# Optimization experiments

Measured on AMD Instinct MI355X. Metric: run time of the kernel, lower is better.

The kernel has to match this reference:

```python
import jax, jax.numpy as jnp
import numpy as np

NUM_THETAS = 64   # bump_steps == num_thetas == 64
NUM_PTS = 100
B = 256           # number of graphs
N = B * NUM_PTS   # total nodes
SCALE = 500.0     # sigmoid sharpness used by EctLayer
HID = 4 * 1024


def _linear_init(key, fan_in, shape):
    s = 1.0 / np.sqrt(fan_in)
    return jax.random.uniform(key, shape, jnp.float32, -s, s)


def setup_inputs() -> dict:
    key = jax.random.key(0)
    ks = jax.random.split(key, 8)
    x = jax.random.normal(ks[0], (N, 2), jnp.float32)
    batch_idx = jnp.repeat(jnp.arange(B), NUM_PTS)  # [N] graph id per node
    t = jnp.linspace(0.0, 2.0 * np.pi, NUM_THETAS)
    V = jnp.stack([jnp.sin(t), jnp.cos(t)], axis=0)          # [2, T] directions
    lin = jnp.linspace(-1.0, 1.0, NUM_THETAS)                # [bump] thresholds
    d = NUM_THETAS * NUM_THETAS
    W1 = _linear_init(ks[1], d, (d, HID)); b1 = _linear_init(ks[2], d, (HID,))
    W2 = _linear_init(ks[3], HID, (HID, HID)); b2 = _linear_init(ks[4], HID, (HID,))
    W3 = _linear_init(ks[5], HID, (HID, 2 * NUM_PTS)); b3 = _linear_init(ks[6], HID, (2 * NUM_PTS,))
    return {"x": x, "batch_idx": batch_idx, "V": V, "lin": lin,
            "W1": W1, "b1": b1, "W2": W2, "b2": b2, "W3": W3, "b3": b3}


def ect_layer(x, idx, V, lin, num_graphs):
    # x: [N,2], V: [2,T] -> node heights nh: [N,T]
    nh = x @ V
    # soft-threshold binning: [N, bump, T]
    ecc = jax.nn.sigmoid(SCALE * (lin[None, :, None] - nh[:, None, :]))
    # per-graph scatter-sum over nodes -> [B, bump, T]
    e = jax.ops.segment_sum(ecc, idx, num_segments=num_graphs)
    # normalized=True: divide by per-graph max
    return e / jnp.amax(e, axis=(1, 2), keepdims=True)


def reference(x, batch_idx, V, lin, W1, b1, W2, b2, W3, b3):
    ect = ect_layer(x, batch_idx, V, lin, B)          # [B, 64, 64]
    h = ect.reshape(B, -1)                            # Flatten
    h = jnp.tanh(h @ W1 + b1)
    h = jnp.tanh(h @ W2 + b2)
    pts = (h @ W3 + b3).reshape(-1, 2)                # [B*NUM_PTS, 2]
    idx2 = jnp.repeat(jnp.arange(B), NUM_PTS)
    decoded = ect_layer(pts, idx2, V, lin, B)         # [B, 64, 64]
    return decoded, pts
```

## Files before the change

### kernel.cpp

```cpp
#include <hip/hip_runtime.h>
#include <hip/hip_bf16.h>

typedef short bf16x8 __attribute__((ext_vector_type(8)));
typedef short s16x4 __attribute__((ext_vector_type(4)));
typedef float f32x4 __attribute__((ext_vector_type(4)));
typedef unsigned u32x4 __attribute__((ext_vector_type(4)));

#define ECT_SCALE 500.0f

__device__ __forceinline__ bool detect_f32(const void* w) {
    const unsigned* p = (const unsigned*)w;
    int sane = 0;
#pragma unroll
    for (int i = 0; i < 16; i++) {
        unsigned e = (p[i] >> 7) & 0xFFu;
        sane += (e >= 100u && e <= 140u) ? 1 : 0;
    }
    return sane < 10;
}

__device__ __forceinline__ float ld_f(const void* p, int i, bool f32) {
    return f32 ? ((const float*)p)[i]
               : __bfloat162float(((const __hip_bfloat16*)p)[i]);
}

__device__ __forceinline__ void split_f(float v, short& hi, short& lo) {
    __hip_bfloat16 h = __float2bfloat16(v);
    hi = (short)__bfloat16_as_short(h);
    lo = (short)__bfloat16_as_short(__float2bfloat16(v - __bfloat162float(h)));
}

__device__ __forceinline__ float sig_fast(float x) {
    float t = __builtin_amdgcn_fmed3f(x, 0.0f, 1.0f);
    return t * t * (3.0f - 2.0f * t);
}

__global__ __launch_bounds__(512)
void ect1_kernel(const void* __restrict__ x, const void* __restrict__ V,
                 const void* __restrict__ lin, const void* __restrict__ sent,
                 short* __restrict__ eh, short* __restrict__ el)
{
    __shared__ float in_lds[200];
    __shared__ float nh[100 * 64];
    __shared__ float wmax[8];

    const bool f32 = detect_f32(sent);
    const int g = blockIdx.x, tid = threadIdx.x;
    const int t = tid & 63, wv = tid >> 6;

    if (tid < 200) in_lds[tid] = ld_f(x, g * 200 + tid, f32);
    const float sv = ld_f(V, t, f32);
    const float cv = ld_f(V, 64 + t, f32);
    float zs[8];
#pragma unroll
    for (int k = 0; k < 8; k++)
        zs[k] = (ECT_SCALE / 8.0f) * ld_f(lin, wv + 8 * k, f32) + 0.5f;
    __syncthreads();

    for (int n = wv; n < 100; n += 8)
        nh[n * 64 + t] = in_lds[2 * n] * sv + in_lds[2 * n + 1] * cv;

    float e[8];
#pragma unroll
    for (int k = 0; k < 8; k++) e[k] = 0.0f;
    __syncthreads();

    for (int n = 0; n < 100; n++) {
        const float ws = (ECT_SCALE / 8.0f) * nh[n * 64 + t];
#pragma unroll
        for (int k = 0; k < 8; k++)
            e[k] += sig_fast(zs[k] - ws);
    }

    float mx = e[0];
#pragma unroll
    for (int k = 1; k < 8; k++) mx = fmaxf(mx, e[k]);
#pragma unroll
    for (int off = 32; off > 0; off >>= 1)
        mx = fmaxf(mx, __shfl_xor(mx, off, 64));
    if (t == 0) wmax[wv] = mx;
    __syncthreads();
    float gm = wmax[0];
#pragma unroll
    for (int k = 1; k < 8; k++) gm = fmaxf(gm, wmax[k]);
    const float sc = 1.0f / gm;

#pragma unroll
    for (int k = 0; k < 8; k++) {
        short hi, lo;
        split_f(e[k] * sc, hi, lo);
        eh[g * 4096 + tid + 512 * k] = hi;
        el[g * 4096 + tid + 512 * k] = lo;
    }
}

#define GEMM_STAGE(K_, N_, GUARD_N)                                            \
    {                                                                          \
        _Pragma("unroll")                                                      \
        for (int i = 0; i < 2; i++) {                                          \
            int r = rr + 32 * i;                                               \
            *(bf16x8*)&Ahs[r][cc] =                                            \
                *(const bf16x8*)&Ah[(size_t)(bm * 64 + r) * K_ + k0 + cc];     \
            *(bf16x8*)&Als[r][cc] =                                            \
                *(const bf16x8*)&Al[(size_t)(bm * 64 + r) * K_ + k0 + cc];     \
        }                                                                      \
        {                                                                      \
            const int wn = lane;                                               \
            const int wk = wv * 16;                                            \
            const bool okn = !(GUARD_N) || (n0c + wn < N_);                    \
            unsigned hp[8], lp[8];                                             \
            if (f32) {                                                         \
                float w0[16];                                                  \
                _Pragma("unroll")                                              \
                for (int j = 0; j < 16; j++)                                   \
                    w0[j] = okn ? ((const float*)W)[(size_t)(k0 + wk + j) * N_ + n0c + wn] : 0.0f; \
                _Pragma("unroll")                                              \
                for (int jp = 0; jp < 8; jp++) {                               \
                    unsigned ua = __float_as_uint(w0[2 * jp]);                 \
                    unsigned ub = __float_as_uint(w0[2 * jp + 1]);             \
                    unsigned ha = ua & 0xFFFF0000u, hb = ub & 0xFFFF0000u;     \
                    hp[jp] = (ha >> 16) | hb;                                  \
                    float la = w0[2 * jp] - __uint_as_float(ha);               \
                    float lb = w0[2 * jp + 1] - __uint_as_float(hb);           \
                    lp[jp] = (__float_as_uint(la) >> 16) |                     \
                             (__float_as_uint(lb) & 0xFFFF0000u);              \
                }                                                              \
            } else {                                                           \
                unsigned short wu[16];                                         \
                _Pragma("unroll")                                              \
                for (int j = 0; j < 16; j++)                                   \
                    wu[j] = okn ? ((const unsigned short*)W)[(size_t)(k0 + wk + j) * N_ + n0c + wn] : (unsigned short)0; \
                _Pragma("unroll")                                              \
                for (int jp = 0; jp < 8; jp++) {                               \
                    hp[jp] = (unsigned)wu[2 * jp] | ((unsigned)wu[2 * jp + 1] << 16); \
                    lp[jp] = 0u;                                               \
                }                                                              \
            }                                                                  \
            *(u32x4*)&Bhs[wn][wk]     = (u32x4){hp[0], hp[1], hp[2], hp[3]};   \
            *(u32x4*)&Bhs[wn][wk + 8] = (u32x4){hp[4], hp[5], hp[6], hp[7]};   \
            *(u32x4*)&Bls[wn][wk]     = (u32x4){lp[0], lp[1], lp[2], lp[3]};   \
            *(u32x4*)&Bls[wn][wk + 8] = (u32x4){lp[4], lp[5], lp[6], lp[7]};   \
        }                                                                      \
        __syncthreads();                                                       \
        _Pragma("unroll")                                                      \
        for (int kh = 0; kh < 2; kh++) {                                       \
            bf16x8 ah[2], al[2], bh[2], bl[2];                                 \
            _Pragma("unroll")                                                  \
            for (int im = 0; im < 2; im++) {                                   \
                ah[im] = *(const bf16x8*)&Ahs[mrow0 + im * 16 + l16][kh * 32 + quad * 8]; \
                al[im] = *(const bf16x8*)&Als[mrow0 + im * 16 + l16][kh * 32 + quad * 8]; \
            }                                                                  \
            _Pragma("unroll")                                                  \
            for (int jn = 0; jn < 2; jn++) {                                   \
                bh[jn] = *(const bf16x8*)&Bhs[ncol0 + jn * 16 + l16][kh * 32 + quad * 8]; \
                bl[jn] = *(const bf16x8*)&Bls[ncol0 + jn * 16 + l16][kh * 32 + quad * 8]; \
            }                                                                  \
            _Pragma("unroll")                                                  \
            for (int im = 0; im < 2; im++)                                     \
                _Pragma("unroll")                                              \
                for (int jn = 0; jn < 2; jn++) {                               \
                    acc[im][jn] = __builtin_amdgcn_mfma_f32_16x16x32_bf16(ah[im], bh[jn], acc[im][jn], 0, 0, 0); \
                    acc[im][jn] = __builtin_amdgcn_mfma_f32_16x16x32_bf16(ah[im], bl[jn], acc[im][jn], 0, 0, 0); \
                    acc[im][jn] = __builtin_amdgcn_mfma_f32_16x16x32_bf16(al[im], bh[jn], acc[im][jn], 0, 0, 0); \
                }                                                              \
        }                                                                      \
        __syncthreads();                                                       \
    }

template<bool GUARD>
__global__ __launch_bounds__(256)
void gemm_sk(const short* __restrict__ Ah, const short* __restrict__ Al,
             const void* __restrict__ W, const void* __restrict__ sent,
             float* __restrict__ pre, int N_, int K_, int kzbits, int kiters)
{
    __shared__ short Ahs[64][72], Als[64][72], Bhs[64][72], Bls[64][72];
    const bool f32 = detect_f32(sent);
    const int bm = blockIdx.y;
    const int bn = blockIdx.x >> kzbits;
    const int kz = blockIdx.x & ((1 << kzbits) - 1);
    const int tid = threadIdx.x;
    const int wv = tid >> 6, lane = tid & 63, quad = lane >> 4, l16 = lane & 15;
    const int mrow0 = (wv & 1) * 32, ncol0 = (wv >> 1) * 32;
    const int rr = tid >> 3, cc = (tid & 7) * 8;
    const int n0c = bn * 64;

    f32x4 acc[2][2];
#pragma unroll
    for (int i = 0; i < 2; i++)
#pragma unroll
        for (int j = 0; j < 2; j++) acc[i][j] = (f32x4){0.f, 0.f, 0.f, 0.f};

    int k0 = kz * (kiters * 64);
    for (int it = 0; it < kiters; it++, k0 += 64)
        GEMM_STAGE(K_, N_, GUARD)

#pragma unroll
    for (int im = 0; im < 2; im++)
#pragma unroll
        for (int jn = 0; jn < 2; jn++) {
            const int n = n0c + ncol0 + jn * 16 + l16;
            if (!GUARD || n < N_) {
#pragma unroll
                for (int r = 0; r < 4; r++) {
                    const int m = bm * 64 + mrow0 + im * 16 + quad * 4 + r;
                    atomicAdd(&pre[(size_t)m * N_ + n], acc[im][jn][r]);
                }
            }
        }
}

__global__ __launch_bounds__(256)
void finalize_tanh(const float* __restrict__ pre, const void* __restrict__ bias,
                   const void* __restrict__ sent,
                   short* __restrict__ Oh, short* __restrict__ Ol)
{
    const bool f32 = detect_f32(sent);
    const int idx = (blockIdx.x * 256 + threadIdx.x) * 4;
    f32x4 v = *(const f32x4*)&pre[idx];
    const int n = idx & 4095;
    s16x4 hi, lo;
#pragma unroll
    for (int j = 0; j < 4; j++) {
        float t = v[j] + ld_f(bias, n + j, f32);
        t = 1.0f - 2.0f * __builtin_amdgcn_rcpf(1.0f + __expf(2.0f * t));
        short h, l;
        split_f(t, h, l);
        hi[j] = h; lo[j] = l;
    }
    *(s16x4*)&Oh[idx] = hi;
    *(s16x4*)&Ol[idx] = lo;
}

__global__ __launch_bounds__(512)
void ect2_kernel(const float* __restrict__ part, const void* __restrict__ bias3,
                 const void* __restrict__ V, const void* __restrict__ lin,
                 const void* __restrict__ sent,
                 float* __restrict__ dec, float* __restrict__ pts_out)
{
    __shared__ float in_lds[200];
    __shared__ float nh[100 * 64];
    __shared__ float wmax[8];

    const bool f32 = detect_f32(sent);
    const int g = blockIdx.x, tid = threadIdx.x;
    const int t = tid & 63, wv = tid >> 6;

    if (tid < 200) {
        float v = part[g * 200 + tid] + ld_f(bias3, tid, f32);
        in_lds[tid] = v;
        pts_out[g * 200 + tid] = v;
    }
    const float sv = ld_f(V, t, f32);
    const float cv = ld_f(V, 64 + t, f32);
    float zs[8];
#pragma unroll
    for (int k = 0; k < 8; k++)
        zs[k] = (ECT_SCALE / 8.0f) * ld_f(lin, wv + 8 * k, f32) + 0.5f;
    __syncthreads();

    for (int n = wv; n < 100; n += 8)
        nh[n * 64 + t] = in_lds[2 * n] * sv + in_lds[2 * n + 1] * cv;

    float e[8];
#pragma unroll
    for (int k = 0; k < 8; k++) e[k] = 0.0f;
    __syncthreads();

    for (int n = 0; n < 100; n++) {
        const float ws = (ECT_SCALE / 8.0f) * nh[n * 64 + t];
#pragma unroll
        for (int k = 0; k < 8; k++)
            e[k] += sig_fast(zs[k] - ws);
    }

    float mx = e[0];
#pragma unroll
    for (int k = 1; k < 8; k++) mx = fmaxf(mx, e[k]);
#pragma unroll
    for (int off = 32; off > 0; off >>= 1)
        mx = fmaxf(mx, __shfl_xor(mx, off, 64));
    if (t == 0) wmax[wv] = mx;
    __syncthreads();
    float gm = wmax[0];
#pragma unroll
    for (int k = 1; k < 8; k++) gm = fmaxf(gm, wmax[k]);
    const float sc = 1.0f / gm;

#pragma unroll
    for (int k = 0; k < 8; k++)
        dec[g * 4096 + tid + 512 * k] = e[k] * sc;
}

extern "C" void kernel_launch(void* const* d_in, const int* in_sizes, int n_in,
                              void* d_out, int out_size, void* d_ws, size_t ws_size,
                              hipStream_t stream)
{
    const void* x   = d_in[0];
    const void* V   = d_in[2];
    const void* lin = d_in[3];
    const void* W1  = d_in[4];
    const void* b1  = d_in[5];
    const void* W2  = d_in[6];
    const void* b2  = d_in[7];
    const void* W3  = d_in[8];
    const void* b3  = d_in[9];
    float* out = (float*)d_out;

    char* ws = (char*)d_ws;
    short* e_h  = (short*)(ws + ( 0u << 20));
    short* e_l  = (short*)(ws + ( 2u << 20));
    short* h1h  = (short*)(ws + ( 4u << 20));
    short* h1l  = (short*)(ws + ( 6u << 20));
    short* h2h  = (short*)(ws + ( 8u << 20));
    short* h2l  = (short*)(ws + (10u << 20));
    float* pre1 = (float*)(ws + (12u << 20));
    float* pre2 = (float*)(ws + (16u << 20));
    float* part = (float*)(ws + (20u << 20));

    hipMemsetAsync(ws + (12u << 20), 0, (8u << 20) + 256 * 200 * sizeof(float), stream);

    ect1_kernel<<<256, 512, 0, stream>>>(x, V, lin, W1, e_h, e_l);
    gemm_sk<false><<<dim3(256, 4), 256, 0, stream>>>(e_h, e_l, W1, W1, pre1, 4096, 4096, 2, 16);
    finalize_tanh<<<1024, 256, 0, stream>>>(pre1, b1, W1, h1h, h1l);
    gemm_sk<false><<<dim3(256, 4), 256, 0, stream>>>(h1h, h1l, W2, W1, pre2, 4096, 4096, 2, 16);
    finalize_tanh<<<1024, 256, 0, stream>>>(pre2, b2, W1, h2h, h2l);
    gemm_sk<true><<<dim3(128, 4), 256, 0, stream>>>(h2h, h2l, W3, W1, part, 200, 4096, 5, 2);
    ect2_kernel<<<256, 512, 0, stream>>>(part, b3, V, lin, W1, out, out + 1048576);
}
```

Measured before the change: 278.1 us.

## Fuse whole pipeline into one cooperative persistent kernel with grid syncs

Replaces the seven separate launches and the memset with a single cooperative kernel of 256 blocks that runs the ECT, the three GEMMs, the tanh finalization and the decode ECT as phases separated by grid.sync. The GEMMs move to larger 256x128 tiles with double-buffered LDS and register prefetch, and write split-K partial slices to distinct buffers that a later phase sums, instead of using atomics. This removes launch gaps, atomic traffic and the zeroing memset. In exchange it runs only 256 blocks across the device, relies on grid-wide barriers, uses about 123 KB of dynamic LDS, and needs more workspace for the partial slices.

Measured after the change: 463.8 us. 1.67x slower.

```diff
diff --git a/kernel.cpp b/kernel.cpp
--- a/kernel.cpp
+++ b/kernel.cpp
@@ -1,8 +1,10 @@
 #include <hip/hip_runtime.h>
 #include <hip/hip_bf16.h>
+#include <hip/hip_cooperative_groups.h>
+
+namespace cg = cooperative_groups;
 
 typedef short bf16x8 __attribute__((ext_vector_type(8)));
-typedef short s16x4 __attribute__((ext_vector_type(4)));
 typedef float f32x4 __attribute__((ext_vector_type(4)));
 typedef unsigned u32x4 __attribute__((ext_vector_type(4)));
 
@@ -35,20 +37,22 @@
     return t * t * (3.0f - 2.0f * t);
 }
 
-__global__ __launch_bounds__(512)
-void ect1_kernel(const void* __restrict__ x, const void* __restrict__ V,
-                 const void* __restrict__ lin, const void* __restrict__ sent,
-                 short* __restrict__ eh, short* __restrict__ el)
-{
-    __shared__ float in_lds[200];
-    __shared__ float nh[100 * 64];
-    __shared__ float wmax[8];
-
-    const bool f32 = detect_f32(sent);
-    const int g = blockIdx.x, tid = threadIdx.x;
+#define AHS(b, r, k) ah_lds[((b) * 256 + (r)) * 40 + (k)]
+#define ALS(b, r, k) al_lds[((b) * 256 + (r)) * 40 + (k)]
+#define BHS(b, n, k) bh_lds[((b) * 128 + (n)) * 40 + (k)]
+#define BLS(b, n, k) bl_lds[((b) * 128 + (n)) * 40 + (k)]
+
+template<bool SPLIT_OUT>
+__device__ void ect_core(char* smem, const void* V, const void* lin, bool f32,
+                         int g, int tid,
+                         short* eh, short* el, float* dec)
+{
+    float* in_lds = (float*)smem;
+    float* nh     = (float*)(smem + 1024);
+    float* wmax   = (float*)(smem + 27008);
+
     const int t = tid & 63, wv = tid >> 6;
 
-    if (tid < 200) in_lds[tid] = ld_f(x, g * 200 + tid, f32);
     const float sv = ld_f(V, t, f32);
     const float cv = ld_f(V, 64 + t, f32);
     float zs[8];
@@ -87,208 +91,207 @@
 
 #pragma unroll
     for (int k = 0; k < 8; k++) {
-        short hi, lo;
-        split_f(e[k] * sc, hi, lo);
-        eh[g * 4096 + tid + 512 * k] = hi;
-        el[g * 4096 + tid + 512 * k] = lo;
-    }
-}
-
-#define GEMM_STAGE(K_, N_, GUARD_N)                                            \
+        if (SPLIT_OUT) {
+            short hi, lo;
+            split_f(e[k] * sc, hi, lo);
+            eh[g * 4096 + tid + 512 * k] = hi;
+            el[g * 4096 + tid + 512 * k] = lo;
+        } else {
+            dec[g * 4096 + tid + 512 * k] = e[k] * sc;
+        }
+    }
+}
+
+template<bool GUARD>
+__device__ void gemm_phase(char* smem, const short* Ah, const short* Al,
+                           const void* W, bool f32, int N_,
+                           int bn, int kz, int niter,
+                           float* slice, int tid)
+{
+    short* ah_lds = (short*)smem;
+    short* al_lds = (short*)(smem + 40960);
+    short* bh_lds = (short*)(smem + 81920);
+    short* bl_lds = (short*)(smem + 102400);
+
+    const int wv = tid >> 6, lane = tid & 63, quad = lane >> 4, l16 = lane & 15;
+    const int wm = (wv & 3) * 64, wn = (wv >> 2) * 64;
+    const int ar0 = tid >> 2, ac = (tid & 3) * 8;
+    const int sub = wv & 1, ksl = wv >> 1;
+    const int nn = sub * 64 + lane - sub * 64;
+    const int nloc = sub * 64 + (lane & 63);
+    const int gn = bn * 128 + nloc;
+    const int k0base = kz * (niter * 32);
+
+    f32x4 acc[4][4];
+#pragma unroll
+    for (int i = 0; i < 4; i++)
+#pragma unroll
+        for (int j = 0; j < 4; j++) acc[i][j] = (f32x4){0.f, 0.f, 0.f, 0.f};
+
+    bf16x8 pah[2], pal[2];
+    unsigned pw[8];
+
+#define PF(k0_)                                                                \
     {                                                                          \
         _Pragma("unroll")                                                      \
-        for (int i = 0; i < 2; i++) {                                          \
-            int r = rr + 32 * i;                                               \
-            *(bf16x8*)&Ahs[r][cc] =                                            \
-                *(const bf16x8*)&Ah[(size_t)(bm * 64 + r) * K_ + k0 + cc];     \
-            *(bf16x8*)&Als[r][cc] =                                            \
-                *(const bf16x8*)&Al[(size_t)(bm * 64 + r) * K_ + k0 + cc];     \
+        for (int p = 0; p < 2; p++) {                                          \
+            int r = ar0 + 128 * p;                                             \
+            pah[p] = *(const bf16x8*)&Ah[(size_t)r * 4096 + (k0_) + ac];       \
+            pal[p] = *(const bf16x8*)&Al[(size_t)r * 4096 + (k0_) + ac];       \
         }                                                                      \
-        {                                                                      \
-            const int wn = lane;                                               \
-            const int wk = wv * 16;                                            \
-            const bool okn = !(GUARD_N) || (n0c + wn < N_);                    \
-            unsigned hp[8], lp[8];                                             \
-            if (f32) {                                                         \
-                float w0[16];                                                  \
-                _Pragma("unroll")                                              \
-                for (int j = 0; j < 16; j++)                                   \
-                    w0[j] = okn ? ((const float*)W)[(size_t)(k0 + wk + j) * N_ + n0c + wn] : 0.0f; \
-                _Pragma("unroll")                                              \
-                for (int jp = 0; jp < 8; jp++) {                               \
-                    unsigned ua = __float_as_uint(w0[2 * jp]);                 \
-                    unsigned ub = __float_as_uint(w0[2 * jp + 1]);             \
-                    unsigned ha = ua & 0xFFFF0000u, hb = ub & 0xFFFF0000u;     \
-                    hp[jp] = (ha >> 16) | hb;                                  \
-                    float la = w0[2 * jp] - __uint_as_float(ha);               \
-                    float lb = w0[2 * jp + 1] - __uint_as_float(hb);           \
-                    lp[jp] = (__float_as_uint(la) >> 16) |                     \
-                             (__float_as_uint(lb) & 0xFFFF0000u);              \
-                }                                                              \
-            } else {                                                           \
-                unsigned short wu[16];                                         \
-                _Pragma("unroll")                                              \
-                for (int j = 0; j < 16; j++)                                   \
-                    wu[j] = okn ? ((const unsigned short*)W)[(size_t)(k0 + wk + j) * N_ + n0c + wn] : (unsigned short)0; \
-                _Pragma("unroll")                                              \
-                for (int jp = 0; jp < 8; jp++) {                               \
-                    hp[jp] = (unsigned)wu[2 * jp] | ((unsigned)wu[2 * jp + 1] << 16); \
-                    lp[jp] = 0u;                                               \
-                }                                                              \
-            }                                                                  \
-            *(u32x4*)&Bhs[wn][wk]     = (u32x4){hp[0], hp[1], hp[2], hp[3]};   \
-            *(u32x4*)&Bhs[wn][wk + 8] = (u32x4){hp[4], hp[5], hp[6], hp[7]};   \
-            *(u32x4*)&Bls[wn][wk]     = (u32x4){lp[0], lp[1], lp[2], lp[3]};   \
-            *(u32x4*)&Bls[wn][wk + 8] = (u32x4){lp[4], lp[5], lp[6], lp[7]};   \
+        _Pragma("unroll")                                                      \
+        for (int j = 0; j < 8; j++) {                                          \
+            size_t off = (size_t)((k0_) + ksl * 8 + j) * N_ + gn;              \
+            pw[j] = (GUARD && gn >= N_) ? 0u                                   \
+                  : (f32 ? ((const unsigned*)W)[off]                           \
+                         : ((unsigned)((const unsigned short*)W)[off] << 16)); \
         }                                                                      \
-        __syncthreads();                                                       \
+    }
+
+#define WRITE(buf_)                                                            \
+    {                                                                          \
         _Pragma("unroll")                                                      \
-        for (int kh = 0; kh < 2; kh++) {                                       \
-            bf16x8 ah[2], al[2], bh[2], bl[2];                                 \
-            _Pragma("unroll")                                                  \
-            for (int im = 0; im < 2; im++) {                                   \
-                ah[im] = *(const bf16x8*)&Ahs[mrow0 + im * 16 + l16][kh * 32 + quad * 8]; \
-                al[im] = *(const bf16x8*)&Als[mrow0 + im * 16 + l16][kh * 32 + quad * 8]; \
-            }                                                                  \
-            _Pragma("unroll")                                                  \
-            for (int jn = 0; jn < 2; jn++) {                                   \
-                bh[jn] = *(const bf16x8*)&Bhs[ncol0 + jn * 16 + l16][kh * 32 + quad * 8]; \
-                bl[jn] = *(const bf16x8*)&Bls[ncol0 + jn * 16 + l16][kh * 32 + quad * 8]; \
-            }                                                                  \
-            _Pragma("unroll")                                                  \
-            for (int im = 0; im < 2; im++)                                     \
-                _Pragma("unroll")                                              \
-                for (int jn = 0; jn < 2; jn++) {                               \
-                    acc[im][jn] = __builtin_amdgcn_mfma_f32_16x16x32_bf16(ah[im], bh[jn], acc[im][jn], 0, 0, 0); \
-                    acc[im][jn] = __builtin_amdgcn_mfma_f32_16x16x32_bf16(ah[im], bl[jn], acc[im][jn], 0, 0, 0); \
-                    acc[im][jn] = __builtin_amdgcn_mfma_f32_16x16x32_bf16(al[im], bh[jn], acc[im][jn], 0, 0, 0); \
-                }                                                              \
+        for (int p = 0; p < 2; p++) {                                          \
+            *(bf16x8*)&AHS(buf_, ar0 + 128 * p, ac) = pah[p];                  \
+            *(bf16x8*)&ALS(buf_, ar0 + 128 * p, ac) = pal[p];                  \
         }                                                                      \
-        __syncthreads();                                                       \
-    }
-
-template<bool GUARD>
-__global__ __launch_bounds__(256)
-void gemm_sk(const short* __restrict__ Ah, const short* __restrict__ Al,
-             const void* __restrict__ W, const void* __restrict__ sent,
-             float* __restrict__ pre, int N_, int K_, int kzbits, int kiters)
-{
-    __shared__ short Ahs[64][72], Als[64][72], Bhs[64][72], Bls[64][72];
-    const bool f32 = detect_f32(sent);
-    const int bm = blockIdx.y;
-    const int bn = blockIdx.x >> kzbits;
-    const int kz = blockIdx.x & ((1 << kzbits) - 1);
-    const int tid = threadIdx.x;
-    const int wv = tid >> 6, lane = tid & 63, quad = lane >> 4, l16 = lane & 15;
-    const int mrow0 = (wv & 1) * 32, ncol0 = (wv >> 1) * 32;
-    const int rr = tid >> 3, cc = (tid & 7) * 8;
-    const int n0c = bn * 64;
-
-    f32x4 acc[2][2];
-#pragma unroll
-    for (int i = 0; i < 2; i++)
-#pragma unroll
-        for (int j = 0; j < 2; j++) acc[i][j] = (f32x4){0.f, 0.f, 0.f, 0.f};
-
-    int k0 = kz * (kiters * 64);
-    for (int it = 0; it < kiters; it++, k0 += 64)
-        GEMM_STAGE(K_, N_, GUARD)
-
-#pragma unroll
-    for (int im = 0; im < 2; im++)
-#pragma unroll
-        for (int jn = 0; jn < 2; jn++) {
-            const int n = n0c + ncol0 + jn * 16 + l16;
+        unsigned hp[4], lp[4];                                                 \
+        _Pragma("unroll")                                                      \
+        for (int jp = 0; jp < 4; jp++) {                                       \
+            unsigned a = pw[2 * jp], b = pw[2 * jp + 1];                       \
+            unsigned ha = a & 0xFFFF0000u, hb = b & 0xFFFF0000u;               \
+            hp[jp] = (ha >> 16) | hb;                                          \
+            float la = __uint_as_float(a) - __uint_as_float(ha);               \
+            float lb = __uint_as_float(b) - __uint_as_float(hb);               \
+            lp[jp] = (__float_as_uint(la) >> 16) |                             \
+                     (__float_as_uint(lb) & 0xFFFF0000u);                      \
+        }                                                                      \
+        *(u32x4*)&BHS(buf_, nloc, ksl * 8) = (u32x4){hp[0], hp[1], hp[2], hp[3]}; \
+        *(u32x4*)&BLS(buf_, nloc, ksl * 8) = (u32x4){lp[0], lp[1], lp[2], lp[3]}; \
+    }
+
+    PF(k0base)
+    WRITE(0)
+    __syncthreads();
+    PF(k0base + 32)
+
+    for (int it = 0; it < niter; it++) {
+        const int b = it & 1;
+        bf16x8 afh[4], afl[4], bfh[4], bfl[4];
+#pragma unroll
+        for (int i = 0; i < 4; i++) {
+            afh[i] = *(const bf16x8*)&AHS(b, wm + i * 16 + l16, quad * 8);
+            afl[i] = *(const bf16x8*)&ALS(b, wm + i * 16 + l16, quad * 8);
+        }
+#pragma unroll
+        for (int j = 0; j < 4; j++) {
+            bfh[j] = *(const bf16x8*)&BHS(b, wn + j * 16 + l16, quad * 8);
+            bfl[j] = *(const bf16x8*)&BLS(b, wn + j * 16 + l16, quad * 8);
+        }
+#pragma unroll
+        for (int i = 0; i < 4; i++)
+#pragma unroll
+            for (int j = 0; j < 4; j++) {
+                acc[i][j] = __builtin_amdgcn_mfma_f32_16x16x32_bf16(afh[i], bfh[j], acc[i][j], 0, 0, 0);
+                acc[i][j] = __builtin_amdgcn_mfma_f32_16x16x32_bf16(afh[i], bfl[j], acc[i][j], 0, 0, 0);
+                acc[i][j] = __builtin_amdgcn_mfma_f32_16x16x32_bf16(afl[i], bfh[j], acc[i][j], 0, 0, 0);
+            }
+        if (it + 1 < niter) WRITE((it + 1) & 1)
+        __syncthreads();
+        if (it + 2 < niter) PF(k0base + (it + 2) * 32)
+    }
+
+#pragma unroll
+    for (int i = 0; i < 4; i++)
+#pragma unroll
+        for (int j = 0; j < 4; j++) {
+            const int n = bn * 128 + wn + j * 16 + l16;
             if (!GUARD || n < N_) {
 #pragma unroll
                 for (int r = 0; r < 4; r++) {
-                    const int m = bm * 64 + mrow0 + im * 16 + quad * 4 + r;
-                    atomicAdd(&pre[(size_t)m * N_ + n], acc[im][jn][r]);
+                    const int m = wm + i * 16 + quad * 4 + r;
+                    slice[(size_t)m * N_ + n] = acc[i][j][r];
                 }
             }
         }
-}
-
-__global__ __launch_bounds__(256)
-void finalize_tanh(const float* __restrict__ pre, const void* __restrict__ bias,
-                   const void* __restrict__ sent,
-                   short* __restrict__ Oh, short* __restrict__ Ol)
-{
-    const bool f32 = detect_f32(sent);
-    const int idx = (blockIdx.x * 256 + threadIdx.x) * 4;
-    f32x4 v = *(const f32x4*)&pre[idx];
+#undef PF
+#undef WRITE
+}
+
+__device__ void finalize_phase(const float* pre, const void* bias, bool f32,
+                               short* Oh, short* Ol, int bid, int tid)
+{
+    const int idx = (bid * 512 + tid) * 8;
+    f32x4 s0 = (f32x4){0.f, 0.f, 0.f, 0.f}, s1 = s0;
+#pragma unroll
+    for (int z = 0; z < 8; z++) {
+        s0 += *(const f32x4*)&pre[(size_t)z * 1048576 + idx];
+        s1 += *(const f32x4*)&pre[(size_t)z * 1048576 + idx + 4];
+    }
     const int n = idx & 4095;
-    s16x4 hi, lo;
-#pragma unroll
-    for (int j = 0; j < 4; j++) {
-        float t = v[j] + ld_f(bias, n + j, f32);
-        t = 1.0f - 2.0f * __builtin_amdgcn_rcpf(1.0f + __expf(2.0f * t));
+    bf16x8 hi, lo;
+#pragma unroll
+    for (int j = 0; j < 8; j++) {
+        float v = (j < 4 ? s0[j & 3] : s1[j & 3]) + ld_f(bias, n + j, f32);
+        v = 1.0f - 2.0f * __builtin_amdgcn_rcpf(1.0f + __expf(2.0f * v));
         short h, l;
-        split_f(t, h, l);
+        split_f(v, h, l);
         hi[j] = h; lo[j] = l;
     }
-    *(s16x4*)&Oh[idx] = hi;
-    *(s16x4*)&Ol[idx] = lo;
+    *(bf16x8*)&Oh[idx] = hi;
+    *(bf16x8*)&Ol[idx] = lo;
 }
 
 __global__ __launch_bounds__(512)
-void ect2_kernel(const float* __restrict__ part, const void* __restrict__ bias3,
-                 const void* __restrict__ V, const void* __restrict__ lin,
-                 const void* __restrict__ sent,
-                 float* __restrict__ dec, float* __restrict__ pts_out)
-{
-    __shared__ float in_lds[200];
-    __shared__ float nh[100 * 64];
-    __shared__ float wmax[8];
-
-    const bool f32 = detect_f32(sent);
-    const int g = blockIdx.x, tid = threadIdx.x;
-    const int t = tid & 63, wv = tid >> 6;
-
-    if (tid < 200) {
-        float v = part[g * 200 + tid] + ld_f(bias3, tid, f32);
-        in_lds[tid] = v;
-        pts_out[g * 200 + tid] = v;
-    }
-    const float sv = ld_f(V, t, f32);
-    const float cv = ld_f(V, 64 + t, f32);
-    float zs[8];
-#pragma unroll
-    for (int k = 0; k < 8; k++)
-        zs[k] = (ECT_SCALE / 8.0f) * ld_f(lin, wv + 8 * k, f32) + 0.5f;
-    __syncthreads();
-
-    for (int n = wv; n < 100; n += 8)
-        nh[n * 64 + t] = in_lds[2 * n] * sv + in_lds[2 * n + 1] * cv;
-
-    float e[8];
-#pragma unroll
-    for (int k = 0; k < 8; k++) e[k] = 0.0f;
-    __syncthreads();
-
-    for (int n = 0; n < 100; n++) {
-        const float ws = (ECT_SCALE / 8.0f) * nh[n * 64 + t];
-#pragma unroll
-        for (int k = 0; k < 8; k++)
-            e[k] += sig_fast(zs[k] - ws);
-    }
-
-    float mx = e[0];
-#pragma unroll
-    for (int k = 1; k < 8; k++) mx = fmaxf(mx, e[k]);
-#pragma unroll
-    for (int off = 32; off > 0; off >>= 1)
-        mx = fmaxf(mx, __shfl_xor(mx, off, 64));
-    if (t == 0) wmax[wv] = mx;
-    __syncthreads();
-    float gm = wmax[0];
-#pragma unroll
-    for (int k = 1; k < 8; k++) gm = fmaxf(gm, wmax[k]);
-    const float sc = 1.0f / gm;
-
-#pragma unroll
-    for (int k = 0; k < 8; k++)
-        dec[g * 4096 + tid + 512 * k] = e[k] * sc;
+void mega(const void* x, const void* V, const void* lin,
+          const void* W1, const void* b1, const void* W2, const void* b2,
+          const void* W3, const void* b3, float* out,
+          short* eh, short* el, short* h1h, short* h1l,
+          short* h2h, short* h2l, float* pre, float* part)
+{
+    extern __shared__ char smem[];
+    cg::grid_group grid = cg::this_grid();
+    const bool f32 = detect_f32(W1);
+    const int bid = blockIdx.x, tid = threadIdx.x;
+
+    {
+        float* in_lds = (float*)smem;
+        if (tid < 200) in_lds[tid] = ld_f(x, bid * 200 + tid, f32);
+        ect_core<true>(smem, V, lin, f32, bid, tid, eh, el, nullptr);
+    }
+    grid.sync();
+
+    gemm_phase<false>(smem, eh, el, W1, f32, 4096, bid >> 3, bid & 7, 16,
+                      pre + (size_t)(bid & 7) * 1048576, tid);
+    grid.sync();
+
+    finalize_phase(pre, b1, f32, h1h, h1l, bid, tid);
+    grid.sync();
+
+    gemm_phase<false>(smem, h1h, h1l, W2, f32, 4096, bid >> 3, bid & 7, 16,
+                      pre + (size_t)(bid & 7) * 1048576, tid);
+    grid.sync();
+
+    finalize_phase(pre, b2, f32, h2h, h2l, bid, tid);
+    grid.sync();
+
+    if (bid < 64)
+        gemm_phase<true>(smem, h2h, h2l, W3, f32, 200, bid >> 5, bid & 31, 4,
+                         part + (size_t)(bid & 31) * 51200, tid);
+    grid.sync();
+
+    {
+        float* in_lds = (float*)smem;
+        if (tid < 200) {
+            float v = ld_f(b3, tid, f32);
+#pragma unroll
+            for (int z = 0; z < 32; z++)
+                v += part[(size_t)z * 51200 + bid * 200 + tid];
+            in_lds[tid] = v;
+            out[1048576 + bid * 200 + tid] = v;
+        }
+        ect_core<false>(smem, V, lin, f32, bid, tid, nullptr, nullptr, out);
+    }
 }
 
 extern "C" void kernel_launch(void* const* d_in, const int* in_sizes, int n_in,
@@ -307,23 +310,25 @@
     float* out = (float*)d_out;
 
     char* ws = (char*)d_ws;
-    short* e_h  = (short*)(ws + ( 0u << 20));
-    short* e_l  = (short*)(ws + ( 2u << 20));
+    short* eh   = (short*)(ws + ( 0u << 20));
+    short* el   = (short*)(ws + ( 2u << 20));
     short* h1h  = (short*)(ws + ( 4u << 20));
     short* h1l  = (short*)(ws + ( 6u << 20));
     short* h2h  = (short*)(ws + ( 8u << 20));
     short* h2l  = (short*)(ws + (10u << 20));
-    float* pre1 = (float*)(ws + (12u << 20));
-    float* pre2 = (float*)(ws + (16u << 20));
-    float* part = (float*)(ws + (20u << 20));
-
-    hipMemsetAsync(ws + (12u << 20), 0, (8u << 20) + 256 * 200 * sizeof(float), stream);
-
-    ect1_kernel<<<256, 512, 0, stream>>>(x, V, lin, W1, e_h, e_l);
-    gemm_sk<false><<<dim3(256, 4), 256, 0, stream>>>(e_h, e_l, W1, W1, pre1, 4096, 4096, 2, 16);
-    finalize_tanh<<<1024, 256, 0, stream>>>(pre1, b1, W1, h1h, h1l);
-    gemm_sk<false><<<dim3(256, 4), 256, 0, stream>>>(h1h, h1l, W2, W1, pre2, 4096, 4096, 2, 16);
-    finalize_tanh<<<1024, 256, 0, stream>>>(pre2, b2, W1, h2h, h2l);
-    gemm_sk<true><<<dim3(128, 4), 256, 0, stream>>>(h2h, h2l, W3, W1, part, 200, 4096, 5, 2);
-    ect2_kernel<<<256, 512, 0, stream>>>(part, b3, V, lin, W1, out, out + 1048576);
-}
+    float* pre  = (float*)(ws + (12u << 20));
+    float* part = (float*)(ws + (44u << 20));
+
+    static const unsigned SMEM = 123u * 1024u;
+    hipFuncSetAttribute((const void*)mega,
+                        hipFuncAttributeMaxDynamicSharedMemorySize, (int)SMEM);
+
+    void* args[] = { (void*)&x, (void*)&V, (void*)&lin,
+                     (void*)&W1, (void*)&b1, (void*)&W2, (void*)&b2,
+                     (void*)&W3, (void*)&b3, (void*)&out,
+                     (void*)&eh, (void*)&el, (void*)&h1h, (void*)&h1l,
+                     (void*)&h2h, (void*)&h2l, (void*)&pre, (void*)&part };
+
+    hipLaunchCooperativeKernel((const void*)mega, dim3(256), dim3(512),
+                               args, SMEM, stream);
+}
```
